# Kernel optimization log

Measured on AMD Instinct MI355X. Metric: run time of the kernel, lower is better.

The kernel has to match this reference:

```python
import jax, jax.numpy as jnp
import numpy as np

TEMPERATURE = 1.0

def setup_inputs() -> dict:
    key = jax.random.key(0)
    k1, k2 = jax.random.split(key)
    z1 = jax.random.normal(k1, (8, 256, 2048), dtype=jnp.float32)
    z2 = jax.random.normal(k2, (8, 256, 2048), dtype=jnp.float32)
    return {"z1": z1, "z2": z2}

def reference(z1, z2):
    # logits[b, n, m] = sum_s z1[b, s, n] * z2[b, s, m], scaled by temperature
    logits = jnp.einsum('bsn,bsm->bnm', z1, z2) / TEMPERATURE
    # torch F.cross_entropy on (b, C=n, m) with labels[b, m] = m:
    # softmax over axis 1 (n), then gather the diagonal n == m.
    logp = jax.nn.log_softmax(logits, axis=1)        # (b, n, m)
    diag = jnp.diagonal(logp, axis1=1, axis2=2)      # (b, m) = logp[b, m, m]
    return -jnp.mean(diag)
```

## Files before the change

kernel.cpp:

```cpp
#include <hip/hip_runtime.h>
#include <hip/hip_bf16.h>


#define NN 2048
#define SK 256
#define LDST 264
#define LOG2E 1.4426950408889634f
#define LN2   0.6931471805599453f
#define COFF  96.0f

typedef __attribute__((ext_vector_type(8))) short short8;
typedef __attribute__((ext_vector_type(16))) float f32x16;

__device__ __forceinline__ unsigned short f2bf(float f) {
    __hip_bfloat16 h = __float2bfloat16(f);
    unsigned short u; __builtin_memcpy(&u, &h, 2); return u;
}

__device__ __forceinline__ float exp2g(float x) {
#if __has_builtin(__builtin_amdgcn_exp2f)
    return __builtin_amdgcn_exp2f(x);
#else
    return exp2f(x);
#endif
}

__device__ __forceinline__ float log2g(float x) {
#if __has_builtin(__builtin_amdgcn_logf)
    return __builtin_amdgcn_logf(x);
#else
    return log2f(x);
#endif
}

__global__ __launch_bounds__(512) void gemm_lse_kernel(
    const float* __restrict__ z1, const float* __restrict__ z2,
    float* __restrict__ ws_sum, float* __restrict__ ws_diag)
{
    __shared__ unsigned short lds[2][32 * LDST];

    const int bid  = blockIdx.x;
    const int b    = bid & 7;
    const int tile = bid >> 3;
    const int mb   = tile & 3;
    const int ns   = tile >> 2;
    const int tid  = threadIdx.x;
    const int lane = tid & 63;
    const int w    = tid >> 6;
    const int col  = lane & 31;
    const int kg   = lane >> 5;

    const int m0      = mb * 512 + w * 64;
    const int mcol0   = m0 + col;
    const int mcol1   = m0 + 32 + col;
    const int n_start = ns * 256;

    const float* z1b = z1 + (size_t)b * SK * NN;
    const float* z2b = z2 + (size_t)b * SK * NN;

    const int kc  = (w << 1) | kg;
    const int row = col;
    float apf[16];
    auto load_A = [&](int t) {
        const float* p = z1b + (size_t)(kc * 16) * NN + (n_start + 32 * t + row);
        #pragma unroll
        for (int j = 0; j < 16; ++j) apf[j] = p[(size_t)j * NN];
    };
    auto store_A = [&](unsigned short* buf) {
        short8 pk0, pk1;
        #pragma unroll
        for (int j = 0; j < 8; ++j) { pk0[j] = (short)f2bf(apf[j]); pk1[j] = (short)f2bf(apf[j + 8]); }
        *(short8*)(buf + row * LDST + kc * 16)     = pk0;
        *(short8*)(buf + row * LDST + kc * 16 + 8) = pk1;
    };

    short8 bf0[16], bf1[16];
    auto loadB = [&](int ks) {
        short8 p0, p1;
        #pragma unroll
        for (int j = 0; j < 8; ++j) {
            const int s = ks * 16 + kg * 8 + j;
            p0[j] = (short)f2bf(z2b[(size_t)s * NN + mcol0] * LOG2E);
            p1[j] = (short)f2bf(z2b[(size_t)s * NN + mcol1] * LOG2E);
        }
        bf0[ks] = p0; bf1[ks] = p1;
    };

    #pragma unroll
    for (int ks = 0; ks < 8; ++ks) loadB(ks);
    load_A(0);
    store_A(lds[0]);
    load_A(1);
    #pragma unroll
    for (int ks = 8; ks < 16; ++ks) loadB(ks);

    float srun0 = 0.0f, srun1 = 0.0f;

    __syncthreads();

    for (int t = 0; t < 8; ++t) {
        const unsigned short* abase = lds[t & 1] + col * LDST + kg * 8;

        f32x16 acc0, acc1;
        #pragma unroll
        for (int r = 0; r < 16; ++r) { acc0[r] = -COFF; acc1[r] = -COFF; }

        #pragma unroll
        for (int ks = 0; ks < 16; ++ks) {
            short8 af = *(const short8*)(abase + ks * 16);
            acc0 = __builtin_amdgcn_mfma_f32_32x32x16_bf16(af, bf0[ks], acc0, 0, 0, 0);
            acc1 = __builtin_amdgcn_mfma_f32_32x32x16_bf16(af, bf1[ks], acc1, 0, 0, 0);
        }

        if (t < 7) store_A(lds[(t + 1) & 1]);
        if (t < 6) load_A(t + 2);

        const int nsub = n_start + 32 * t;
        if (nsub == m0) {
            #pragma unroll
            for (int r = 0; r < 16; ++r) {
                const int rw = (r & 3) + 8 * (r >> 2) + 4 * kg;
                if (rw == col) ws_diag[b * NN + mcol0] = acc0[r];
            }
        }
        if (nsub == m0 + 32) {
            #pragma unroll
            for (int r = 0; r < 16; ++r) {
                const int rw = (r & 3) + 8 * (r >> 2) + 4 * kg;
                if (rw == col) ws_diag[b * NN + mcol1] = acc1[r];
            }
        }

        {
            float e0 = 0, e1 = 0, e2 = 0, e3 = 0;
            #pragma unroll
            for (int r = 0; r < 16; r += 4) {
                e0 += exp2g(acc0[r]);     e1 += exp2g(acc0[r + 1]);
                e2 += exp2g(acc0[r + 2]); e3 += exp2g(acc0[r + 3]);
            }
            srun0 += (e0 + e1) + (e2 + e3);
        }
        {
            float e0 = 0, e1 = 0, e2 = 0, e3 = 0;
            #pragma unroll
            for (int r = 0; r < 16; r += 4) {
                e0 += exp2g(acc1[r]);     e1 += exp2g(acc1[r + 1]);
                e2 += exp2g(acc1[r + 2]); e3 += exp2g(acc1[r + 3]);
            }
            srun1 += (e0 + e1) + (e2 + e3);
        }

        __syncthreads();
    }

    srun0 += __shfl_xor(srun0, 32);
    srun1 += __shfl_xor(srun1, 32);
    if (kg == 0) {
        ws_sum[(b * 8 + ns) * NN + mcol0] = srun0;
        ws_sum[(b * 8 + ns) * NN + mcol1] = srun1;
    }
}

__global__ __launch_bounds__(256) void merge_kernel(
    const float* __restrict__ ws_sum, const float* __restrict__ ws_diag,
    float* __restrict__ partial)
{
    const int gid = blockIdx.x * 256 + threadIdx.x;
    const int b = gid >> 11, m = gid & (NN - 1);

    float S = 0.0f;
    #pragma unroll
    for (int slot = 0; slot < 8; ++slot)
        S += ws_sum[(b * 8 + slot) * NN + m];
    float c = log2g(S) - ws_diag[gid];

    #pragma unroll
    for (int d = 1; d < 64; d <<= 1) c += __shfl_xor(c, d);
    __shared__ float red[4];
    if ((threadIdx.x & 63) == 0) red[threadIdx.x >> 6] = c;
    __syncthreads();
    if (threadIdx.x == 0)
        partial[blockIdx.x] = red[0] + red[1] + red[2] + red[3];
}

__global__ void final_kernel(const float* __restrict__ partial, float* __restrict__ out)
{
    float v = partial[threadIdx.x];
    #pragma unroll
    for (int d = 1; d < 64; d <<= 1) v += __shfl_xor(v, d);
    if (threadIdx.x == 0) out[0] = v * (LN2 / 16384.0f);
}

extern "C" void kernel_launch(void* const* d_in, const int* in_sizes, int n_in,
                              void* d_out, int out_size, void* d_ws, size_t ws_size,
                              hipStream_t stream)
{
    const float* z1 = (const float*)d_in[0];
    const float* z2 = (const float*)d_in[1];
    float* ws  = (float*)d_ws;
    float* out = (float*)d_out;

    float* ws_sum  = ws;
    float* ws_diag = ws + 131072;
    float* ws_part = ws + 147456;

    gemm_lse_kernel<<<dim3(256), dim3(512), 0, stream>>>(z1, z2, ws_sum, ws_diag);
    merge_kernel<<<dim3(64), dim3(256), 0, stream>>>(ws_sum, ws_diag, ws_part);
    final_kernel<<<dim3(1), dim3(64), 0, stream>>>(ws_part, out);
}
```

Baseline: 30.13 us.

## Software-pipeline exp2 epilogue of previous tile under current tile's MFMAs

Double-buffers the MFMA accumulators across the fully unrolled n-tile loop so that the exp2 sum and diagonal extraction of tile t-1 are interleaved with the MFMA chain of tile t. The aim is to hide the transcendental/VALU epilogue behind matrix-core work instead of running the two back to back. In exchange it holds two more 16-float accumulators live, which raises VGPR pressure at 512 threads, and it fully unrolls the tile loop, which grows the code.

```diff
diff --git a/kernel.cpp b/kernel.cpp
--- a/kernel.cpp
+++ b/kernel.cpp
@@ -95,62 +95,83 @@
     for (int ks = 8; ks < 16; ++ks) loadB(ks);
 
     float srun0 = 0.0f, srun1 = 0.0f;
+    f32x16 accE0, accE1, accO0, accO1;
 
     __syncthreads();
 
-    for (int t = 0; t < 8; ++t) {
-        const unsigned short* abase = lds[t & 1] + col * LDST + kg * 8;
-
-        f32x16 acc0, acc1;
-        #pragma unroll
-        for (int r = 0; r < 16; ++r) { acc0[r] = -COFF; acc1[r] = -COFF; }
-
-        #pragma unroll
-        for (int ks = 0; ks < 16; ++ks) {
-            short8 af = *(const short8*)(abase + ks * 16);
-            acc0 = __builtin_amdgcn_mfma_f32_32x32x16_bf16(af, bf0[ks], acc0, 0, 0, 0);
-            acc1 = __builtin_amdgcn_mfma_f32_32x32x16_bf16(af, bf1[ks], acc1, 0, 0, 0);
-        }
-
-        if (t < 7) store_A(lds[(t + 1) & 1]);
-        if (t < 6) load_A(t + 2);
-
-        const int nsub = n_start + 32 * t;
-        if (nsub == m0) {
+#define TILE_BODY(T, CUR0, CUR1, PRV0, PRV1, DOP)                                    \
+    {                                                                                \
+        const unsigned short* abase = lds[(T) & 1] + col * LDST + kg * 8;            \
+        _Pragma("unroll")                                                            \
+        for (int r = 0; r < 16; ++r) { CUR0[r] = -COFF; CUR1[r] = -COFF; }           \
+        float f0 = 0, f1 = 0, g0 = 0, g1 = 0;                                        \
+        _Pragma("unroll")                                                            \
+        for (int ks = 0; ks < 16; ++ks) {                                            \
+            short8 af = *(const short8*)(abase + ks * 16);                           \
+            CUR0 = __builtin_amdgcn_mfma_f32_32x32x16_bf16(af, bf0[ks], CUR0, 0, 0, 0); \
+            CUR1 = __builtin_amdgcn_mfma_f32_32x32x16_bf16(af, bf1[ks], CUR1, 0, 0, 0); \
+            if (DOP) {                                                               \
+                if (ks & 1) { f1 += exp2g(PRV0[ks]); g1 += exp2g(PRV1[ks]); }        \
+                else        { f0 += exp2g(PRV0[ks]); g0 += exp2g(PRV1[ks]); }        \
+            }                                                                        \
+        }                                                                            \
+        if (DOP) { srun0 += f0 + f1; srun1 += g0 + g1; }                             \
+        if (DOP) {                                                                   \
+            const int nsubP = n_start + 32 * ((T) - 1);                              \
+            if (nsubP == m0) {                                                       \
+                _Pragma("unroll")                                                    \
+                for (int r = 0; r < 16; ++r) {                                       \
+                    const int rw = (r & 3) + 8 * (r >> 2) + 4 * kg;                  \
+                    if (rw == col) ws_diag[b * NN + mcol0] = PRV0[r];                \
+                }                                                                    \
+            }                                                                        \
+            if (nsubP == m0 + 32) {                                                  \
+                _Pragma("unroll")                                                    \
+                for (int r = 0; r < 16; ++r) {                                       \
+                    const int rw = (r & 3) + 8 * (r >> 2) + 4 * kg;                  \
+                    if (rw == col) ws_diag[b * NN + mcol1] = PRV1[r];                \
+                }                                                                    \
+            }                                                                        \
+        }                                                                            \
+        if ((T) < 7) store_A(lds[((T) + 1) & 1]);                                    \
+        if ((T) < 6) load_A((T) + 2);                                                \
+        __syncthreads();                                                             \
+    }
+
+    TILE_BODY(0, accE0, accE1, accO0, accO1, false)
+    TILE_BODY(1, accO0, accO1, accE0, accE1, true)
+    TILE_BODY(2, accE0, accE1, accO0, accO1, true)
+    TILE_BODY(3, accO0, accO1, accE0, accE1, true)
+    TILE_BODY(4, accE0, accE1, accO0, accO1, true)
+    TILE_BODY(5, accO0, accO1, accE0, accE1, true)
+    TILE_BODY(6, accE0, accE1, accO0, accO1, true)
+    TILE_BODY(7, accO0, accO1, accE0, accE1, true)
+#undef TILE_BODY
+
+    {
+        float f0 = 0, f1 = 0, g0 = 0, g1 = 0;
+        #pragma unroll
+        for (int r = 0; r < 16; r += 2) {
+            f0 += exp2g(accO0[r]); f1 += exp2g(accO0[r + 1]);
+            g0 += exp2g(accO1[r]); g1 += exp2g(accO1[r + 1]);
+        }
+        srun0 += f0 + f1; srun1 += g0 + g1;
+
+        const int nsubP = n_start + 32 * 7;
+        if (nsubP == m0) {
             #pragma unroll
             for (int r = 0; r < 16; ++r) {
                 const int rw = (r & 3) + 8 * (r >> 2) + 4 * kg;
-                if (rw == col) ws_diag[b * NN + mcol0] = acc0[r];
+                if (rw == col) ws_diag[b * NN + mcol0] = accO0[r];
             }
         }
-        if (nsub == m0 + 32) {
+        if (nsubP == m0 + 32) {
             #pragma unroll
             for (int r = 0; r < 16; ++r) {
                 const int rw = (r & 3) + 8 * (r >> 2) + 4 * kg;
-                if (rw == col) ws_diag[b * NN + mcol1] = acc1[r];
+                if (rw == col) ws_diag[b * NN + mcol1] = accO1[r];
             }
         }
-
-        {
-            float e0 = 0, e1 = 0, e2 = 0, e3 = 0;
-            #pragma unroll
-            for (int r = 0; r < 16; r += 4) {
-                e0 += exp2g(acc0[r]);     e1 += exp2g(acc0[r + 1]);
-                e2 += exp2g(acc0[r + 2]); e3 += exp2g(acc0[r + 3]);
-            }
-            srun0 += (e0 + e1) + (e2 + e3);
-        }
-        {
-            float e0 = 0, e1 = 0, e2 = 0, e3 = 0;
-            #pragma unroll
-            for (int r = 0; r < 16; r += 4) {
-                e0 += exp2g(acc1[r]);     e1 += exp2g(acc1[r + 1]);
-                e2 += exp2g(acc1[r + 2]); e3 += exp2g(acc1[r + 3]);
-            }
-            srun1 += (e0 + e1) + (e2 + e3);
-        }
-
-        __syncthreads();
     }
 
     srun0 += __shfl_xor(srun0, 32);
```

Result: slower. 76.30 us (+153.3%).

## Stage entire A tile in LDS upfront and drop per-iteration barriers

Applied to the files above, without the earlier changes.

Instead of double-buffering 32-row slices of z1 through LDS with a barrier every iteration, each block now loads and converts all 256 rows of its A tile into a single large LDS buffer before the compute loop. The main loop then runs without __syncthreads or interleaved global loads, and is unrolled by 2. This removes per-iteration synchronisation and load/store interleaving. In exchange it raises LDS use to about 135 KB per block and loses the overlap of A loads with MFMA work.

```diff
diff --git a/kernel.cpp b/kernel.cpp
--- a/kernel.cpp
+++ b/kernel.cpp
@@ -37,7 +37,7 @@
     const float* __restrict__ z1, const float* __restrict__ z2,
     float* __restrict__ ws_sum, float* __restrict__ ws_diag)
 {
-    __shared__ unsigned short lds[2][32 * LDST];
+    __shared__ unsigned short lds[256 * LDST];
 
     const int bid  = blockIdx.x;
     const int b    = bid & 7;
@@ -60,22 +60,25 @@
 
     const int kc  = (w << 1) | kg;
     const int row = col;
-    float apf[16];
-    auto load_A = [&](int t) {
-        const float* p = z1b + (size_t)(kc * 16) * NN + (n_start + 32 * t + row);
-        #pragma unroll
-        for (int j = 0; j < 16; ++j) apf[j] = p[(size_t)j * NN];
-    };
-    auto store_A = [&](unsigned short* buf) {
+    #pragma unroll
+    for (int rg = 0; rg < 8; ++rg) {
+        const int nrow = rg * 32 + row;
+        const float* p = z1b + (size_t)(kc * 16) * NN + (n_start + nrow);
+        float t0[8], t1[8];
+        #pragma unroll
+        for (int j = 0; j < 8; ++j) t0[j] = p[(size_t)j * NN];
+        #pragma unroll
+        for (int j = 0; j < 8; ++j) t1[j] = p[(size_t)(j + 8) * NN];
         short8 pk0, pk1;
         #pragma unroll
-        for (int j = 0; j < 8; ++j) { pk0[j] = (short)f2bf(apf[j]); pk1[j] = (short)f2bf(apf[j + 8]); }
-        *(short8*)(buf + row * LDST + kc * 16)     = pk0;
-        *(short8*)(buf + row * LDST + kc * 16 + 8) = pk1;
-    };
+        for (int j = 0; j < 8; ++j) { pk0[j] = (short)f2bf(t0[j]); pk1[j] = (short)f2bf(t1[j]); }
+        *(short8*)(lds + nrow * LDST + kc * 16)     = pk0;
+        *(short8*)(lds + nrow * LDST + kc * 16 + 8) = pk1;
+    }
 
     short8 bf0[16], bf1[16];
-    auto loadB = [&](int ks) {
+    #pragma unroll
+    for (int ks = 0; ks < 16; ++ks) {
         short8 p0, p1;
         #pragma unroll
         for (int j = 0; j < 8; ++j) {
@@ -84,22 +87,15 @@
             p1[j] = (short)f2bf(z2b[(size_t)s * NN + mcol1] * LOG2E);
         }
         bf0[ks] = p0; bf1[ks] = p1;
-    };
-
-    #pragma unroll
-    for (int ks = 0; ks < 8; ++ks) loadB(ks);
-    load_A(0);
-    store_A(lds[0]);
-    load_A(1);
-    #pragma unroll
-    for (int ks = 8; ks < 16; ++ks) loadB(ks);
+    }
 
     float srun0 = 0.0f, srun1 = 0.0f;
 
     __syncthreads();
 
-    for (int t = 0; t < 8; ++t) {
-        const unsigned short* abase = lds[t & 1] + col * LDST + kg * 8;
+    #pragma unroll 2
+    for (int sub = 0; sub < 8; ++sub) {
+        const unsigned short* abase = lds + (32 * sub + col) * LDST + kg * 8;
 
         f32x16 acc0, acc1;
         #pragma unroll
@@ -112,10 +108,7 @@
             acc1 = __builtin_amdgcn_mfma_f32_32x32x16_bf16(af, bf1[ks], acc1, 0, 0, 0);
         }
 
-        if (t < 7) store_A(lds[(t + 1) & 1]);
-        if (t < 6) load_A(t + 2);
-
-        const int nsub = n_start + 32 * t;
+        const int nsub = n_start + 32 * sub;
         if (nsub == m0) {
             #pragma unroll
             for (int r = 0; r < 16; ++r) {
@@ -149,8 +142,6 @@
             }
             srun1 += (e0 + e1) + (e2 + e3);
         }
-
-        __syncthreads();
     }
 
     srun0 += __shfl_xor(srun0, 32);
```

After: 29.15 us (median of 2 runs). 3.2% less time.
